# Kernel optimization log

Measured on AMD Instinct MI355X. Metric: run time of the kernel, lower is better.

The kernel has to match this reference:

```python
import jax, jax.numpy as jnp
import numpy as np

B, S, U, H = 4, 1024, 1024, 16
D = U // H  # d_k = 64


def setup_inputs() -> dict:
    key = jax.random.key(0)
    ks = jax.random.split(key, 11)
    f = lambda k, sh: jax.random.normal(k, sh, dtype=jnp.float32) * 0.02
    # causal multiplicative mask, as commonly passed to this module
    mask = jnp.broadcast_to(jnp.tril(jnp.ones((S, S), jnp.float32)), (B, S, S))
    return {
        "query": f(ks[0], (B, S, U)),
        "key": f(ks[1], (B, S, U)),
        "value": f(ks[2], (B, S, U)),
        "mask": mask,
        "Wq": f(ks[3], (U, U)), "bq": jnp.zeros((U,), jnp.float32),
        "Wk": f(ks[4], (U, U)), "bk": jnp.zeros((U,), jnp.float32),
        "Wv": f(ks[5], (U, U)), "bv": jnp.zeros((U,), jnp.float32),
        "Wo": f(ks[6], (U, U)), "bo": jnp.zeros((U,), jnp.float32),
    }


def reference(query, key, value, mask, Wq, bq, Wk, bk, Wv, bv, Wo, bo):
    scale = 1.0 / np.sqrt(D).astype(np.float32)
    # project and split heads: torch's split(d_k,dim=2)+cat(dim=0) == reshape [B,S,H,D]
    def heads(x, W, b):
        return (x @ W + b).reshape(B, S, H, D)
    q = heads(query, Wq, bq)
    k = heads(key, Wk, bk)
    v = heads(value, Wv, bv)
    A = jnp.einsum('bqhd,bkhd->bhqk', q, k) * scale  # [B,H,S,S]
    m = mask[:, None, :, :]  # broadcast over heads (== mask.repeat(n_heads,1,1))
    A = A * m - 1e10 * (1.0 - m)  # multiplicative + additive masking
    A = jax.nn.softmax(A, axis=-1)
    # dropout p=0.0 -> identity
    out = jnp.einsum('bhqk,bkhd->bqhd', A, v).reshape(B, S, U)
    return out @ Wo + bo
```

## Files before the change

### kernel.cpp

```cpp
#include <hip/hip_runtime.h>
#include <hip/hip_bf16.h>

typedef unsigned short u16;
typedef __attribute__((ext_vector_type(8))) short bf16x8;
typedef __attribute__((ext_vector_type(4))) float f32x4;
constexpr size_t M1 = 1024 * 1024;

static __device__ __forceinline__ float bf2f(u16 u) {
    return __uint_as_float(((unsigned)u) << 16);
}
static __device__ __forceinline__ u16 f2bf(float f) {
    __hip_bfloat16 h = __float2bfloat16(f);
    return *reinterpret_cast<u16*>(&h);
}
static __device__ __forceinline__ void g2lds16(const void* g, void* l) {
    __builtin_amdgcn_global_load_lds(
        (const __attribute__((address_space(1))) unsigned int*)g,
        (__attribute__((address_space(3))) unsigned int*)l, 16, 0, 0);
}
static __device__ __forceinline__ f32x4 mfma16(bf16x8 a, bf16x8 b, f32x4 c) {
    return __builtin_amdgcn_mfma_f32_16x16x32_bf16(a, b, c, 0, 0, 0);
}
static __device__ __forceinline__ bf16x8 ldfrag(const u16* base, int chunk) {
    return *(const bf16x8*)((const char*)base + (size_t)chunk * 16);
}
static __device__ __forceinline__ float fexp2(float x) {
    return __builtin_amdgcn_exp2f(x);
}

static __device__ __forceinline__ bool sniffDev(const u16* __restrict__ qs) {
    const int e = (qs[threadIdx.x & 63] >> 7) & 0xFF;
    return __popcll(__ballot(e >= 130)) >= 2;
}

struct Prep {
    const void* wsrc[4]; u16* wdst[4];
    const float* csrc[3]; u16* cdst[3]; int nCast;
};

__global__ __launch_bounds__(256) void prep_kernel(Prep pa, const u16* __restrict__ qs) {
    const bool f = sniffDev(qs);
    const int tid = threadIdx.x;
    if (blockIdx.z < 4) {
        __shared__ u16 Ts[64][72];
        const void* src = pa.wsrc[blockIdx.z];
        u16* dst = pa.wdst[blockIdx.z];
        const int r0 = blockIdx.x * 64;
        const int c0 = blockIdx.y * 64;
#pragma unroll
        for (int i = 0; i < 4; ++i) {
            const int idx = tid + i * 256;
            const int r = idx >> 4, c4 = (idx & 15) * 4;
            if (f) {
                const float4 v = *(const float4*)((const float*)src + (size_t)(r0 + r) * 1024 + c0 + c4);
                Ts[r][c4 + 0] = f2bf(v.x); Ts[r][c4 + 1] = f2bf(v.y);
                Ts[r][c4 + 2] = f2bf(v.z); Ts[r][c4 + 3] = f2bf(v.w);
            } else {
                const ushort4 v = *(const ushort4*)((const u16*)src + (size_t)(r0 + r) * 1024 + c0 + c4);
                Ts[r][c4 + 0] = v.x; Ts[r][c4 + 1] = v.y;
                Ts[r][c4 + 2] = v.z; Ts[r][c4 + 3] = v.w;
            }
        }
        __syncthreads();
#pragma unroll
        for (int i = 0; i < 4; ++i) {
            const int idx = tid + i * 256;
            const int r = idx >> 4, c4 = (idx & 15) * 4;
            ushort4 o;
            o.x = Ts[c4 + 0][r]; o.y = Ts[c4 + 1][r];
            o.z = Ts[c4 + 2][r]; o.w = Ts[c4 + 3][r];
            *(ushort4*)(dst + (size_t)(c0 + r) * 1024 + r0 + c4) = o;
        }
    } else {
        if (!f) return;
        const int bid = (blockIdx.z - 4) * 256 + blockIdx.y * 16 + blockIdx.x;
        const int total = pa.nCast * 524288;
        for (int c = bid * 256 + tid; c < total; c += 1024 * 256) {
            const int t = c >> 19;
            const size_t off = (size_t)(c & 524287);
            const float4 v0 = *((const float4*)pa.csrc[t] + off * 2);
            const float4 v1 = *((const float4*)pa.csrc[t] + off * 2 + 1);
            int4 v; u16* pv = (u16*)&v;
            pv[0] = f2bf(v0.x); pv[1] = f2bf(v0.y); pv[2] = f2bf(v0.z); pv[3] = f2bf(v0.w);
            pv[4] = f2bf(v1.x); pv[5] = f2bf(v1.y); pv[6] = f2bf(v1.z); pv[7] = f2bf(v1.w);
            *((int4*)pa.cdst[t] + off) = v;
        }
    }
}

struct G1 { const void* X; const u16* Xc; const u16* Wt; const void* Bias; void* Y; int yMode; };
struct G3 { G1 g[3]; };

union GS8 {
    struct { u16 A[2][2][128 * 64]; u16 B[2][2][128 * 64]; } st;
    u16 C[256 * 256];
};

__global__ __launch_bounds__(512, 2) void gemm256(
    G3 args, const u16* __restrict__ qs)
{
    __shared__ __align__(16) GS8 sm;
    const G1 g = args.g[blockIdx.z];
    const bool f = sniffDev(qs);
    const bool regA = f && (g.Xc == nullptr);
    const int tid = threadIdx.x;
    const int lane = tid & 63, w = tid >> 6;
    const int quad = lane >> 4, l16 = lane & 15;
    const int wr = w >> 2, wc = w & 3;
    const int rowBase = blockIdx.x * 256, colBase = blockIdx.y * 256;

    const u16* Xb = f ? g.Xc : (const u16*)g.X;
    const float* Xf = (const float*)g.X;

    f32x4 acc[8][4];
#pragma unroll
    for (int i = 0; i < 8; ++i)
#pragma unroll
        for (int j = 0; j < 4; ++j)
            acc[i][j] = f32x4{0.f, 0.f, 0.f, 0.f};

    auto stA = [&](int bf2, int h, int T2) {
        if (!regA) {
#pragma unroll
            for (int c = 0; c < 2; ++c) {
                const int l = c * 512 + tid;
                const int r  = ((l >> 6) << 3) | (l & 7);
                const int kc = (l >> 3) & 7;
                g2lds16(Xb + (size_t)(rowBase + h * 128 + r) * 1024 + T2 * 64 + kc * 8,
                        (char*)sm.st.A[bf2][h] + (size_t)l * 16);
            }
        } else {
#pragma unroll
            for (int c = 0; c < 2; ++c) {
                const int l = c * 512 + tid;
                const int r  = ((l >> 6) << 3) | (l & 7);
                const int kc = (l >> 3) & 7;
                const float* p = Xf + (size_t)(rowBase + h * 128 + r) * 1024 + T2 * 64 + kc * 8;
                const float4 v0 = *(const float4*)p;
                const float4 v1 = *(const float4*)(p + 4);
                int4 v; u16* pv = (u16*)&v;
                pv[0] = f2bf(v0.x); pv[1] = f2bf(v0.y); pv[2] = f2bf(v0.z); pv[3] = f2bf(v0.w);
                pv[4] = f2bf(v1.x); pv[5] = f2bf(v1.y); pv[6] = f2bf(v1.z); pv[7] = f2bf(v1.w);
                *(int4*)((char*)sm.st.A[bf2][h] + (size_t)l * 16) = v;
            }
            __builtin_amdgcn_s_waitcnt(0xC07F);
        }
    };
    auto stB = [&](int bf2, int h, int T2) {
#pragma unroll
        for (int c = 0; c < 2; ++c) {
            const int l = c * 512 + tid;
            const int r  = ((l >> 6) << 3) | (l & 7);
            const int kc = (l >> 3) & 7;
            g2lds16(g.Wt + (size_t)(colBase + h * 128 + r) * 1024 + T2 * 64 + kc * 8,
                    (char*)sm.st.B[bf2][h] + (size_t)l * 16);
        }
    };

    stA(0, 0, 0); stA(0, 1, 0); stB(0, 0, 0); stB(0, 1, 0);
    stA(1, 0, 1); stA(1, 1, 1); stB(1, 0, 1); stB(1, 1, 1);
    if (regA) __builtin_amdgcn_s_waitcnt(0x0074);
    else      __builtin_amdgcn_s_waitcnt(0x0078);
    __builtin_amdgcn_s_barrier();

    bf16x8 a[4][2], b[4][2];
    const int rbB = (wc & 1) * 64;

#pragma unroll 1
    for (int T = 0; T < 16; ++T) {
        const int buf = T & 1, nb = buf ^ 1;
        const u16* Ab = sm.st.A[buf][wr];
        const u16* Bb = sm.st.B[buf][wc >> 1];

#pragma unroll
        for (int i = 0; i < 4; ++i)
#pragma unroll
            for (int ks = 0; ks < 2; ++ks) {
                const int rl = i * 16 + l16;
                a[i][ks] = ldfrag(Ab, ((rl >> 3) << 6) | ((ks * 4 + quad) << 3) | (rl & 7));
            }
#pragma unroll
        for (int j = 0; j < 2; ++j)
#pragma unroll
            for (int ks = 0; ks < 2; ++ks) {
                const int rl = rbB + j * 16 + l16;
                b[j][ks] = ldfrag(Bb, ((rl >> 3) << 6) | ((ks * 4 + quad) << 3) | (rl & 7));
            }
        if (T >= 1 && T <= 14) stA(nb, 0, T + 1);
        __builtin_amdgcn_s_barrier();
        __builtin_amdgcn_s_setprio(1);
#pragma unroll
        for (int ks = 0; ks < 2; ++ks)
#pragma unroll
            for (int i = 0; i < 4; ++i)
#pragma unroll
                for (int j = 0; j < 2; ++j)
                    acc[i][j] = mfma16(a[i][ks], b[j][ks], acc[i][j]);
        __builtin_amdgcn_s_setprio(0);
        __builtin_amdgcn_s_barrier();

#pragma unroll
        for (int j = 2; j < 4; ++j)
#pragma unroll
            for (int ks = 0; ks < 2; ++ks) {
                const int rl = rbB + j * 16 + l16;
                b[j][ks] = ldfrag(Bb, ((rl >> 3) << 6) | ((ks * 4 + quad) << 3) | (rl & 7));
            }
        if (T >= 1 && T <= 14) stA(nb, 1, T + 1);
        __builtin_amdgcn_s_barrier();
        __builtin_amdgcn_s_setprio(1);
#pragma unroll
        for (int ks = 0; ks < 2; ++ks)
#pragma unroll
            for (int i = 0; i < 4; ++i)
#pragma unroll
                for (int j = 2; j < 4; ++j)
                    acc[i][j] = mfma16(a[i][ks], b[j][ks], acc[i][j]);
        __builtin_amdgcn_s_setprio(0);
        __builtin_amdgcn_s_barrier();

#pragma unroll
        for (int i = 0; i < 4; ++i)
#pragma unroll
            for (int ks = 0; ks < 2; ++ks) {
                const int rl = (i + 4) * 16 + l16;
                a[i][ks] = ldfrag(Ab, ((rl >> 3) << 6) | ((ks * 4 + quad) << 3) | (rl & 7));
            }
        if (T <= 13) stB(buf, 0, T + 2);
        __builtin_amdgcn_s_barrier();
        __builtin_amdgcn_s_setprio(1);
#pragma unroll
        for (int ks = 0; ks < 2; ++ks)
#pragma unroll
            for (int i = 0; i < 4; ++i)
#pragma unroll
                for (int j = 2; j < 4; ++j)
                    acc[i + 4][j] = mfma16(a[i][ks], b[j][ks], acc[i + 4][j]);
        __builtin_amdgcn_s_setprio(0);
        __builtin_amdgcn_s_barrier();

        if (T <= 13) stB(buf, 1, T + 2);
        __builtin_amdgcn_s_barrier();
        __builtin_amdgcn_s_setprio(1);
#pragma unroll
        for (int ks = 0; ks < 2; ++ks)
#pragma unroll
            for (int i = 0; i < 4; ++i)
#pragma unroll
                for (int j = 0; j < 2; ++j)
                    acc[i + 4][j] = mfma16(a[i][ks], b[j][ks], acc[i + 4][j]);
        __builtin_amdgcn_s_setprio(0);
        if (T < 14) __builtin_amdgcn_s_waitcnt(0x0074);
        else        __builtin_amdgcn_s_waitcnt(0x0070);
        __builtin_amdgcn_s_barrier();
    }

    const bool yf = (g.yMode == 2) && f;
    if (yf) {
#pragma unroll
        for (int j = 0; j < 4; ++j) {
            const int col = colBase + wc * 64 + j * 16 + l16;
            const float bv = ((const float*)g.Bias)[col];
#pragma unroll
            for (int i = 0; i < 8; ++i)
#pragma unroll
                for (int reg = 0; reg < 4; ++reg) {
                    const int row = rowBase + wr * 128 + i * 16 + quad * 4 + reg;
                    ((float*)g.Y)[(size_t)row * 1024 + col] = acc[i][j][reg] + bv;
                }
        }
        return;
    }

    __syncthreads();
    const bool vmode = (g.yMode == 1);
#pragma unroll
    for (int j = 0; j < 4; ++j) {
        const int cl = wc * 64 + j * 16 + l16;
        const float bv = f ? ((const float*)g.Bias)[colBase + cl]
                           : bf2f(((const u16*)g.Bias)[colBase + cl]);
#pragma unroll
        for (int i = 0; i < 8; ++i)
#pragma unroll
            for (int reg = 0; reg < 4; ++reg) {
                const int rl = wr * 128 + i * 16 + quad * 4 + reg;
                const int R = vmode ? cl : rl;
                const int Cc = vmode ? rl : cl;
                const int idx = R * 256 + ((((Cc >> 3) ^ (R & 31)) << 3) | (Cc & 7));
                sm.C[idx] = f2bf(acc[i][j][reg] + bv);
            }
    }
    __syncthreads();

    const int rr = tid >> 1, half = tid & 1;
    u16* dst;
    if (vmode) {
        const int bb = rowBase >> 10, s0 = rowBase & 1023;
        dst = (u16*)g.Y + (size_t)bb * M1 + (size_t)(colBase + rr) * 1024 + s0 + half * 128;
    } else {
        dst = (u16*)g.Y + (size_t)(rowBase + rr) * 1024 + colBase + half * 128;
    }
#pragma unroll
    for (int k2 = 0; k2 < 16; ++k2) {
        const int chunk = half * 16 + k2;
        const int4 v = *(const int4*)(sm.C + rr * 256 + ((chunk ^ (rr & 31)) << 3));
        *(int4*)(dst + k2 * 8) = v;
    }
}

union GSMem {
    struct { u16 A[3][128 * 32]; u16 B[3][128 * 32]; } st;
    u16 C[128 * 128];
};

__global__ __launch_bounds__(256) void gemm_mfma(
    G3 args, const u16* __restrict__ qs, int xRaw)
{
    __shared__ __align__(16) GSMem sm;
    const G1 g = args.g[blockIdx.z];
    const bool f  = sniffDev(qs);
    const bool xf = xRaw && f;
    const int tid = threadIdx.x;
    const int lane = tid & 63, w = tid >> 6;
    const int quad = lane >> 4, l16 = lane & 15;
    const int wm = (w & 1) * 64, wn = (w >> 1) * 64;
    const int rowBase = blockIdx.x * 128, colBase = blockIdx.y * 128;

    const u16* Xp = (const u16*)g.X;
    const float* Xf = (const float*)g.X;

    f32x4 acc[4][4];
#pragma unroll
    for (int i = 0; i < 4; ++i)
#pragma unroll
        for (int j = 0; j < 4; ++j)
            acc[i][j] = f32x4{0.f, 0.f, 0.f, 0.f};

    auto stage = [&](int buf, int k0) {
#pragma unroll
        for (int c = 0; c < 2; ++c) {
            const int l = c * 256 + tid;
            const int r = ((l >> 5) << 3) | (l & 7);
            const int kc = (l >> 3) & 3;
            g2lds16(g.Wt + (size_t)(colBase + r) * 1024 + k0 + kc * 8,
                    (char*)sm.st.B[buf] + (size_t)l * 16);
        }
        if (!xf) {
#pragma unroll
            for (int c = 0; c < 2; ++c) {
                const int l = c * 256 + tid;
                const int r = ((l >> 5) << 3) | (l & 7);
                const int kc = (l >> 3) & 3;
                g2lds16(Xp + (size_t)(rowBase + r) * 1024 + k0 + kc * 8,
                        (char*)sm.st.A[buf] + (size_t)l * 16);
            }
        } else {
#pragma unroll
            for (int c = 0; c < 2; ++c) {
                const int l = c * 256 + tid;
                const int r = ((l >> 5) << 3) | (l & 7);
                const int kc = (l >> 3) & 3;
                const float* p = Xf + (size_t)(rowBase + r) * 1024 + k0 + kc * 8;
                const float4 v0 = *(const float4*)p;
                const float4 v1 = *(const float4*)(p + 4);
                int4 v;
                u16* pv = (u16*)&v;
                pv[0] = f2bf(v0.x); pv[1] = f2bf(v0.y); pv[2] = f2bf(v0.z); pv[3] = f2bf(v0.w);
                pv[4] = f2bf(v1.x); pv[5] = f2bf(v1.y); pv[6] = f2bf(v1.z); pv[7] = f2bf(v1.w);
                *(int4*)((char*)sm.st.A[buf] + (size_t)l * 16) = v;
            }
        }
    };

    auto compute = [&](int buf) {
        bf16x8 a[4], b[4];
#pragma unroll
        for (int i = 0; i < 4; ++i) {
            const int r = wm + i * 16 + l16;
            a[i] = ldfrag(sm.st.A[buf], ((r >> 3) << 5) | (quad << 3) | (r & 7));
        }
#pragma unroll
        for (int j = 0; j < 4; ++j) {
            const int r = wn + j * 16 + l16;
            b[j] = ldfrag(sm.st.B[buf], ((r >> 3) << 5) | (quad << 3) | (r & 7));
        }
#pragma unroll
        for (int i = 0; i < 4; ++i)
#pragma unroll
            for (int j = 0; j < 4; ++j)
                acc[i][j] = mfma16(a[i], b[j], acc[i][j]);
    };

    stage(0, 0);
    stage(1, 32);
#pragma unroll 1
    for (int t = 0; t < 31; ++t) {
        __builtin_amdgcn_s_waitcnt(0x0074);
        __builtin_amdgcn_s_barrier();
        if (t + 2 < 32) stage((t + 2) % 3, (t + 2) * 32);
        compute(t % 3);
    }
    __builtin_amdgcn_s_waitcnt(0x0070);
    __builtin_amdgcn_s_barrier();
    compute(31 % 3);

    const bool yf = (g.yMode == 2) && f;
    if (yf) {
#pragma unroll
        for (int j = 0; j < 4; ++j) {
            const int col = colBase + wn + j * 16 + l16;
            const float bv = ((const float*)g.Bias)[col];
#pragma unroll
            for (int i = 0; i < 4; ++i)
#pragma unroll
                for (int reg = 0; reg < 4; ++reg) {
                    const int row = rowBase + wm + i * 16 + quad * 4 + reg;
                    ((float*)g.Y)[(size_t)row * 1024 + col] = acc[i][j][reg] + bv;
                }
        }
        return;
    }

    __syncthreads();
    const bool vmode = (g.yMode == 1);
#pragma unroll
    for (int j = 0; j < 4; ++j) {
        const int cl = wn + j * 16 + l16;
        const float bv = f ? ((const float*)g.Bias)[colBase + cl]
                           : bf2f(((const u16*)g.Bias)[colBase + cl]);
#pragma unroll
        for (int i = 0; i < 4; ++i)
#pragma unroll
            for (int reg = 0; reg < 4; ++reg) {
                const int rl = wm + i * 16 + quad * 4 + reg;
                const int R = vmode ? cl : rl;
                const int Cc = vmode ? rl : cl;
                const int idx = R * 128 + ((((Cc >> 3) ^ (R & 15)) << 3) | (Cc & 7));
                sm.C[idx] = f2bf(acc[i][j][reg] + bv);
            }
    }
    __syncthreads();

    const int rr = tid >> 1, half = tid & 1;
    u16* dst;
    if (vmode) {
        const int bb = rowBase >> 10, s0 = rowBase & 1023;
        dst = (u16*)g.Y + (size_t)bb * M1 + (size_t)(colBase + rr) * 1024 + s0 + half * 64;
    } else {
        dst = (u16*)g.Y + (size_t)(rowBase + rr) * 1024 + colBase + half * 64;
    }
#pragma unroll
    for (int k2 = 0; k2 < 8; ++k2) {
        const int chunk = half * 8 + k2;
        const int4 v = *(const int4*)(sm.C + rr * 128 + ((chunk ^ (rr & 15)) << 3));
        *(int4*)(dst + k2 * 8) = v;
    }
}

static __device__ __forceinline__ void attn_strip(
    const u16* __restrict__ Ks, const u16* __restrict__ Vs,
    u16* __restrict__ psw, const bf16x8* aq,
    float* m_run, float* l_run, f32x4* O,
    int w, int quad, int l16, bool diag)
{
    f32x4 s[4];
    __builtin_amdgcn_s_setprio(1);
#pragma unroll
    for (int j = 0; j < 4; ++j) {
        const int r = j * 16 + l16;
        const bf16x8 b0 = ldfrag(Ks, ((r >> 3) << 6) | (quad << 3) | (r & 7));
        const bf16x8 b1 = ldfrag(Ks, ((r >> 3) << 6) | ((4 + quad) << 3) | (r & 7));
        f32x4 z = f32x4{0.f, 0.f, 0.f, 0.f};
        z = mfma16(aq[0], b0, z);
        s[j] = mfma16(aq[1], b1, z);
    }
    __builtin_amdgcn_s_setprio(0);

    const float SC2 = 0.125f * 1.44269504089f;
    const int qrow0 = w * 16 + quad * 4;
#pragma unroll
    for (int j = 0; j < 4; ++j) {
        const int key = j * 16 + l16;
#pragma unroll
        for (int reg = 0; reg < 4; ++reg) {
            float v = s[j][reg] * SC2;
            if (diag && key > qrow0 + reg) v = -1e30f;
            s[j][reg] = v;
        }
    }

    float alpha[4];
#pragma unroll
    for (int reg = 0; reg < 4; ++reg) {
        float mx = fmaxf(fmaxf(s[0][reg], s[1][reg]), fmaxf(s[2][reg], s[3][reg]));
#pragma unroll
        for (int d = 1; d < 16; d <<= 1)
            mx = fmaxf(mx, __shfl_xor(mx, d));
        const float m_new = fmaxf(m_run[reg], mx);
        alpha[reg] = fexp2(m_run[reg] - m_new);
        float sm = 0.f;
#pragma unroll
        for (int j = 0; j < 4; ++j) {
            const float p = fexp2(s[j][reg] - m_new);
            s[j][reg] = p;
            sm += p;
        }
#pragma unroll
        for (int d = 1; d < 16; d <<= 1)
            sm += __shfl_xor(sm, d);
        l_run[reg] = l_run[reg] * alpha[reg] + sm;
        m_run[reg] = m_new;
    }

#pragma unroll
    for (int j = 0; j < 4; ++j)
#pragma unroll
        for (int reg = 0; reg < 4; ++reg)
            psw[(quad * 4 + reg) * 72 + j * 16 + l16] = f2bf(s[j][reg]);

#pragma unroll
    for (int j = 0; j < 4; ++j)
#pragma unroll
        for (int reg = 0; reg < 4; ++reg)
            O[j][reg] *= alpha[reg];

    bf16x8 ap[2];
#pragma unroll
    for (int kt = 0; kt < 2; ++kt)
        ap[kt] = *(const bf16x8*)((const char*)psw + (size_t)l16 * 144 + kt * 64 + quad * 16);
    __builtin_amdgcn_s_setprio(1);
#pragma unroll
    for (int j = 0; j < 4; ++j) {
        const int r = j * 16 + l16;
        const bf16x8 b0 = ldfrag(Vs, ((r >> 3) << 6) | (quad << 3) | (r & 7));
        const bf16x8 b1 = ldfrag(Vs, ((r >> 3) << 6) | ((4 + quad) << 3) | (r & 7));
        O[j] = mfma16(ap[0], b0, O[j]);
        O[j] = mfma16(ap[1], b1, O[j]);
    }
    __builtin_amdgcn_s_setprio(0);
}

__global__ __launch_bounds__(256) void attn_mfma(
    u16* __restrict__ qw, const u16* __restrict__ kw, const u16* __restrict__ vt)
{
    __shared__ __align__(16) u16 QA[64 * 64];
    __shared__ __align__(16) u16 QB[64 * 64];
    __shared__ __align__(16) u16 Ks[2][64 * 64];
    __shared__ __align__(16) u16 Vs[2][64 * 64];
    __shared__ __align__(16) u16 Ps[4][16 * 72];

    const int tid = threadIdx.x;
    const int lane = tid & 63, w = tid >> 6;
    const int quad = lane >> 4, l16 = lane & 15;
    const int qp = blockIdx.x, bh = blockIdx.y;
    const int b = bh >> 4, h = bh & 15;
    const int qtA = qp, qtB = 15 - qp;

    const u16* qgA = qw + (size_t)(b * 1024 + qtA * 64) * 1024 + h * 64;
    const u16* qgB = qw + (size_t)(b * 1024 + qtB * 64) * 1024 + h * 64;
    const u16* kg0 = kw + (size_t)(b * 1024) * 1024 + h * 64;
    const u16* vg0 = vt + (size_t)b * M1 + (size_t)(h * 64) * 1024;

    auto stageKV = [&](int buf, int kb) {
#pragma unroll
        for (int c = 0; c < 2; ++c) {
            const int l = c * 256 + tid;
            const int r = ((l >> 6) << 3) | (l & 7);
            const int kc = (l >> 3) & 7;
            g2lds16(kg0 + (size_t)(kb + r) * 1024 + kc * 8, (char*)Ks[buf] + (size_t)l * 16);
            g2lds16(vg0 + (size_t)r * 1024 + kb + kc * 8,   (char*)Vs[buf] + (size_t)l * 16);
        }
    };

#pragma unroll
    for (int c = 0; c < 2; ++c) {
        const int l = c * 256 + tid;
        const int r = ((l >> 6) << 3) | (l & 7);
        const int kc = (l >> 3) & 7;
        g2lds16(qgA + (size_t)r * 1024 + kc * 8, (char*)QA + (size_t)l * 16);
        g2lds16(qgB + (size_t)r * 1024 + kc * 8, (char*)QB + (size_t)l * 16);
    }
    stageKV(0, 0);
    __syncthreads();

    bf16x8 aqA[2], aqB[2];
    {
        const int r = w * 16 + l16;
#pragma unroll
        for (int kt = 0; kt < 2; ++kt) {
            aqA[kt] = ldfrag(QA, ((r >> 3) << 6) | ((kt * 4 + quad) << 3) | (r & 7));
            aqB[kt] = ldfrag(QB, ((r >> 3) << 6) | ((kt * 4 + quad) << 3) | (r & 7));
        }
    }

    f32x4 OA[4], OB[4];
    float mA[4], lA[4], mB[4], lB[4];
#pragma unroll
    for (int j = 0; j < 4; ++j) {
        OA[j] = f32x4{0.f, 0.f, 0.f, 0.f};
        OB[j] = f32x4{0.f, 0.f, 0.f, 0.f};
        mA[j] = -1e30f; lA[j] = 0.f;
        mB[j] = -1e30f; lB[j] = 0.f;
    }
    u16* psw = Ps[w];

    int cur = 0;
    for (int t = 0; t <= qtB; ++t) {
        if (t < qtB) stageKV(cur ^ 1, (t + 1) * 64);
        attn_strip(Ks[cur], Vs[cur], psw, aqB, mB, lB, OB, w, quad, l16, t == qtB);
        if (t <= qtA)
            attn_strip(Ks[cur], Vs[cur], psw, aqA, mA, lA, OA, w, quad, l16, t == qtA);
        __syncthreads();
        cur ^= 1;
    }

#pragma unroll
    for (int half = 0; half < 2; ++half) {
        const int qt = half ? qtB : qtA;
        const float* lr = half ? lB : lA;
        const f32x4* O = half ? OB : OA;
        u16* og = qw + (size_t)(b * 1024 + qt * 64 + w * 16 + quad * 4) * 1024 + h * 64;
#pragma unroll
        for (int reg = 0; reg < 4; ++reg) {
            const float inv = 1.f / lr[reg];
#pragma unroll
            for (int j = 0; j < 4; ++j)
                og[(size_t)reg * 1024 + j * 16 + l16] = f2bf(O[j][reg] * inv);
        }
    }
}

extern "C" void kernel_launch(void* const* d_in, const int* in_sizes, int n_in,
                              void* d_out, int out_size, void* d_ws, size_t ws_size,
                              hipStream_t stream)
{
    const void* query = d_in[0];
    const void* key   = d_in[1];
    const void* value = d_in[2];
    const void* Wq = d_in[4];
    const void* bq = d_in[5];
    const void* Wk = d_in[6];
    const void* bk = d_in[7];
    const void* Wv = d_in[8];
    const void* bv = d_in[9];
    const void* Wo = d_in[10];
    const void* bo = d_in[11];

    u16* qw   = (u16*)d_ws;
    u16* kw   = qw + 4 * M1;
    u16* vt   = qw + 8 * M1;
    u16* wt_o = qw + 12 * M1;
    u16* wt_q = qw + 13 * M1;
    u16* wt_k = qw + 14 * M1;
    u16* wt_v = qw + 15 * M1;

    const bool wsBig = ws_size >= 2 * (20 * M1 + 64);
    u16* xv = wsBig ? (qw + 16 * M1 + 64) : nullptr;

    u16* xq = (u16*)d_out;
    u16* xk = xq + 4 * M1;

    const u16* qs = (const u16*)query;

    Prep pa;
    pa.wsrc[0] = Wq; pa.wsrc[1] = Wk; pa.wsrc[2] = Wv; pa.wsrc[3] = Wo;
    pa.wdst[0] = wt_q; pa.wdst[1] = wt_k; pa.wdst[2] = wt_v; pa.wdst[3] = wt_o;
    pa.csrc[0] = (const float*)query; pa.csrc[1] = (const float*)key;
    pa.csrc[2] = (const float*)value;
    pa.cdst[0] = xq; pa.cdst[1] = xk; pa.cdst[2] = xv;
    pa.nCast = wsBig ? 3 : 2;
    prep_kernel<<<dim3(16, 16, 8), 256, 0, stream>>>(pa, qs);

    G3 qkv;
    qkv.g[0] = G1{query, xq, wt_q, bq, qw, 0};
    qkv.g[1] = G1{key,   xk, wt_k, bk, kw, 0};
    qkv.g[2] = G1{value, xv, wt_v, bv, vt, 1};
    gemm256<<<dim3(16, 4, 3), 512, 0, stream>>>(qkv, qs);

    attn_mfma<<<dim3(8, 64), 256, 0, stream>>>(qw, kw, vt);

    G3 og;
    og.g[0] = G1{qw, nullptr, wt_o, bo, d_out, 2};
    og.g[1] = og.g[0]; og.g[2] = og.g[0];
    gemm_mfma<<<dim3(32, 8, 1), 256, 0, stream>>>(og, qs, 0);
}
```

Baseline: 234.4 us.

## Swizzle GEMM block order, vectorize transposed epilogue stores, lazy softmax rescale

Remaps block indices in both GEMM kernels so consecutively scheduled blocks share operand tiles, improving L2 reuse across XCDs. The V-transposed epilogue now writes four bf16 values as one 64-bit LDS store instead of four scalar stores. In attention, the online softmax skips the running-max update and the O/l rescale unless some lane's new max exceeds the old one by more than 8 (log2 units), which drops exponentials and multiplies but lets unnormalized values grow up to 2^8.

Result: no change. 233.0 us (-0.6%).

```diff
diff --git a/kernel.cpp b/kernel.cpp
--- a/kernel.cpp
+++ b/kernel.cpp
@@ -100,14 +100,17 @@
     G3 args, const u16* __restrict__ qs)
 {
     __shared__ __align__(16) GS8 sm;
-    const G1 g = args.g[blockIdx.z];
+    const int g0 = (blockIdx.z << 6) | (blockIdx.y << 4) | blockIdx.x;
+    const int gs = (g0 & 7) * 24 + (g0 >> 3);
+    const int zb = gs / 64, yb = (gs >> 4) & 3, xb = gs & 15;
+    const G1 g = args.g[zb];
     const bool f = sniffDev(qs);
     const bool regA = f && (g.Xc == nullptr);
     const int tid = threadIdx.x;
     const int lane = tid & 63, w = tid >> 6;
     const int quad = lane >> 4, l16 = lane & 15;
     const int wr = w >> 2, wc = w & 3;
-    const int rowBase = blockIdx.x * 256, colBase = blockIdx.y * 256;
+    const int rowBase = xb * 256, colBase = yb * 256;
 
     const u16* Xb = f ? g.Xc : (const u16*)g.X;
     const float* Xf = (const float*)g.X;
@@ -274,21 +277,40 @@
 
     __syncthreads();
     const bool vmode = (g.yMode == 1);
-#pragma unroll
-    for (int j = 0; j < 4; ++j) {
-        const int cl = wc * 64 + j * 16 + l16;
-        const float bv = f ? ((const float*)g.Bias)[colBase + cl]
-                           : bf2f(((const u16*)g.Bias)[colBase + cl]);
-#pragma unroll
-        for (int i = 0; i < 8; ++i)
-#pragma unroll
-            for (int reg = 0; reg < 4; ++reg) {
-                const int rl = wr * 128 + i * 16 + quad * 4 + reg;
-                const int R = vmode ? cl : rl;
-                const int Cc = vmode ? rl : cl;
-                const int idx = R * 256 + ((((Cc >> 3) ^ (R & 31)) << 3) | (Cc & 7));
-                sm.C[idx] = f2bf(acc[i][j][reg] + bv);
-            }
+    if (vmode) {
+#pragma unroll
+        for (int j = 0; j < 4; ++j) {
+            const int cl = wc * 64 + j * 16 + l16;
+            const float bv = f ? ((const float*)g.Bias)[colBase + cl]
+                               : bf2f(((const u16*)g.Bias)[colBase + cl]);
+            const int R = cl;
+#pragma unroll
+            for (int i = 0; i < 8; ++i) {
+                const int Cc0 = wr * 128 + i * 16 + quad * 4;
+                const int idx0 = R * 256 + ((((Cc0 >> 3) ^ (R & 31)) << 3) | (Cc0 & 7));
+                u16 t4[4];
+#pragma unroll
+                for (int reg = 0; reg < 4; ++reg)
+                    t4[reg] = f2bf(acc[i][j][reg] + bv);
+                *(unsigned long long*)(sm.C + idx0) = *(const unsigned long long*)t4;
+            }
+        }
+    } else {
+#pragma unroll
+        for (int j = 0; j < 4; ++j) {
+            const int cl = wc * 64 + j * 16 + l16;
+            const float bv = f ? ((const float*)g.Bias)[colBase + cl]
+                               : bf2f(((const u16*)g.Bias)[colBase + cl]);
+#pragma unroll
+            for (int i = 0; i < 8; ++i)
+#pragma unroll
+                for (int reg = 0; reg < 4; ++reg) {
+                    const int R = wr * 128 + i * 16 + quad * 4 + reg;
+                    const int Cc = cl;
+                    const int idx = R * 256 + ((((Cc >> 3) ^ (R & 31)) << 3) | (Cc & 7));
+                    sm.C[idx] = f2bf(acc[i][j][reg] + bv);
+                }
+        }
     }
     __syncthreads();
 
@@ -324,7 +346,9 @@
     const int lane = tid & 63, w = tid >> 6;
     const int quad = lane >> 4, l16 = lane & 15;
     const int wm = (w & 1) * 64, wn = (w >> 1) * 64;
-    const int rowBase = blockIdx.x * 128, colBase = blockIdx.y * 128;
+    const int g0 = blockIdx.y * 32 + blockIdx.x;
+    const int gsw = ((g0 & 7) << 5) + (g0 >> 3);
+    const int rowBase = (gsw & 31) * 128, colBase = (gsw >> 5) * 128;
 
     const u16* Xp = (const u16*)g.X;
     const float* Xf = (const float*)g.X;
@@ -489,27 +513,42 @@
         }
     }
 
-    float alpha[4];
+    float mx4[4];
+    float need = -1e30f;
 #pragma unroll
     for (int reg = 0; reg < 4; ++reg) {
         float mx = fmaxf(fmaxf(s[0][reg], s[1][reg]), fmaxf(s[2][reg], s[3][reg]));
 #pragma unroll
         for (int d = 1; d < 16; d <<= 1)
             mx = fmaxf(mx, __shfl_xor(mx, d));
-        const float m_new = fmaxf(m_run[reg], mx);
-        alpha[reg] = fexp2(m_run[reg] - m_new);
+        mx4[reg] = mx;
+        need = fmaxf(need, mx - m_run[reg]);
+    }
+    if (!__all(need <= 8.f)) {
+#pragma unroll
+        for (int reg = 0; reg < 4; ++reg) {
+            const float m_new = fmaxf(m_run[reg], mx4[reg]);
+            const float alpha = fexp2(m_run[reg] - m_new);
+            l_run[reg] *= alpha;
+            m_run[reg] = m_new;
+#pragma unroll
+            for (int j = 0; j < 4; ++j)
+                O[j][reg] *= alpha;
+        }
+    }
+#pragma unroll
+    for (int reg = 0; reg < 4; ++reg) {
         float sm = 0.f;
 #pragma unroll
         for (int j = 0; j < 4; ++j) {
-            const float p = fexp2(s[j][reg] - m_new);
+            const float p = fexp2(s[j][reg] - m_run[reg]);
             s[j][reg] = p;
             sm += p;
         }
 #pragma unroll
         for (int d = 1; d < 16; d <<= 1)
             sm += __shfl_xor(sm, d);
-        l_run[reg] = l_run[reg] * alpha[reg] + sm;
-        m_run[reg] = m_new;
+        l_run[reg] += sm;
     }
 
 #pragma unroll
@@ -517,12 +556,6 @@
 #pragma unroll
         for (int reg = 0; reg < 4; ++reg)
             psw[(quad * 4 + reg) * 72 + j * 16 + l16] = f2bf(s[j][reg]);
-
-#pragma unroll
-    for (int j = 0; j < 4; ++j)
-#pragma unroll
-        for (int reg = 0; reg < 4; ++reg)
-            O[j][reg] *= alpha[reg];
 
     bf16x8 ap[2];
 #pragma unroll
```
